# Performance work log

Hardware: AMD Instinct MI355X
Metric: run time of the kernel (lower is better)

## Reference

```python
import jax, jax.numpy as jnp
import numpy as np

B, S, D, H = 4, 1024, 1024, 16
HD = D // H  # 64
NEG = -10000000.0


def setup_inputs() -> dict:
    key = jax.random.key(0)
    ks = jax.random.split(key, 8)
    x = jax.random.normal(ks[0], (B, S, D), dtype=jnp.float32)
    adj = jax.random.randint(ks[1], (B, S, S), 0, 2).astype(jnp.float32)
    scale = 1.0 / np.sqrt(D)
    Wq = jax.random.normal(ks[2], (D, D), dtype=jnp.float32) * scale
    bq = jnp.zeros((D,), dtype=jnp.float32)
    Wk = jax.random.normal(ks[3], (D, D), dtype=jnp.float32) * scale
    bk = jnp.zeros((D,), dtype=jnp.float32)
    Wv = jax.random.normal(ks[4], (D, D), dtype=jnp.float32) * scale
    bv = jnp.zeros((D,), dtype=jnp.float32)
    return {"x": x, "adj": adj, "Wq": Wq, "bq": bq, "Wk": Wk, "bk": bk, "Wv": Wv, "bv": bv}


def reference(x, adj, Wq, bq, Wk, bk, Wv, bv):
    # QKV projections, split into heads: [B,S,D] -> [B,H,S,HD]
    def heads(t):
        return t.reshape(B, S, H, HD).transpose(0, 2, 1, 3)

    q = heads(x @ Wq + bq)
    k = heads(x @ Wk + bk)
    v = heads(x @ Wv + bv)

    # scaled scores [B,H,S,S]
    scores = jnp.einsum('bhqd,bhkd->bhqk', q, k) / jnp.sqrt(jnp.asarray(HD, x.dtype))
    # adjacency mask: 0 where adj>=0.5 else -1e7, broadcast over heads
    mask_add = jnp.where(adj < 0.5, jnp.asarray(NEG, x.dtype), jnp.asarray(0.0, x.dtype))
    scores = scores + mask_add[:, None, :, :]

    probs = jax.nn.softmax(scores, axis=-1)
    ctx = jnp.einsum('bhqk,bhkd->bhqd', probs, v)  # [B,H,S,HD]
    ctx = ctx.transpose(0, 2, 1, 3).reshape(B, S, D)
    h = jax.nn.relu(ctx)
    return (h, adj)
```

## Files before the change

### kernel.cpp

```cpp
#include <hip/hip_runtime.h>

constexpr int Bn  = 4;
constexpr int Sn  = 1024;
constexpr int Dn  = 1024;
constexpr int Hn  = 16;
constexpr int HDn = 64;

using short8   = __attribute__((ext_vector_type(8))) short;
using float4v  = __attribute__((ext_vector_type(4))) float;
using float16v = __attribute__((ext_vector_type(16))) float;

__device__ __forceinline__ ushort f2bf(float f) {
    union { float f; unsigned u; } v; v.f = f;
    unsigned r = v.u + 0x7fff + ((v.u >> 16) & 1);
    return (ushort)(r >> 16);
}

__device__ __forceinline__ void gload16(const void* g, void* l) {
    __builtin_amdgcn_global_load_lds(
        (const __attribute__((address_space(1))) void*)g,
        (__attribute__((address_space(3))) void*)l, 16, 0, 0);
}

__global__ __launch_bounds__(256) void prep(
    const float* __restrict__ x,
    const float* __restrict__ Wq, const float* __restrict__ Wk,
    const float* __restrict__ Wv, const float* __restrict__ adj,
    ushort* __restrict__ xb, ushort* __restrict__ Wt, uint* __restrict__ Mb,
    float* __restrict__ out)
{
    const int bx  = blockIdx.x;
    const int tid = threadIdx.x;
    __shared__ __align__(16) ushort pool[64 * 72];

    if (bx < 2048) {
        const size_t i = ((size_t)bx * 256 + tid) * 8;
        float4 a = *(const float4*)&x[i];
        float4 b = *(const float4*)&x[i + 4];
        ushort o[8] = {f2bf(a.x), f2bf(a.y), f2bf(a.z), f2bf(a.w),
                       f2bf(b.x), f2bf(b.y), f2bf(b.z), f2bf(b.w)};
        *(uint4*)&xb[i] = *(const uint4*)o;
    } else if (bx < 2816) {
        const int idx = bx - 2048;
        const int which = idx >> 8, rem = idx & 255;
        const float* __restrict__ W = (which == 0) ? Wq : (which == 1) ? Wk : Wv;
        ushort* __restrict__ O = Wt + (size_t)which * Dn * Dn;
        const int k0 = (rem & 15) * 64, n0 = (rem >> 4) * 64;
        ushort* T = pool;

        const int kl = tid >> 4, nl = (tid & 15) * 4;
#pragma unroll
        for (int p = 0; p < 4; ++p) {
            float4 w4 = *(const float4*)&W[(size_t)(k0 + p * 16 + kl) * Dn + n0 + nl];
            T[(nl + 0) * 72 + p * 16 + kl] = f2bf(w4.x);
            T[(nl + 1) * 72 + p * 16 + kl] = f2bf(w4.y);
            T[(nl + 2) * 72 + p * 16 + kl] = f2bf(w4.z);
            T[(nl + 3) * 72 + p * 16 + kl] = f2bf(w4.w);
        }
        __syncthreads();
        const int nr = tid >> 2, kc = (tid & 3) * 16;
        uint4 u0 = *(const uint4*)&T[nr * 72 + kc];
        uint4 u1 = *(const uint4*)&T[nr * 72 + kc + 8];
        *(uint4*)&O[(size_t)(n0 + nr) * Dn + k0 + kc]     = u0;
        *(uint4*)&O[(size_t)(n0 + nr) * Dn + k0 + kc + 8] = u1;
    } else {
        const int idx = bx - 2816;
        const int kt = idx & 15, qt = (idx >> 4) & 7, b = idx >> 7;
        char* msk = (char*)pool;

        float* ocopy = out + (size_t)Bn * Sn * Dn;
        const int r16 = tid >> 4, c4 = (tid & 15) * 4;
#pragma unroll
        for (int p = 0; p < 8; ++p) {
            const int row = p * 16 + r16;
            const size_t gi = ((size_t)b * Sn + qt * 128 + row) * Sn + kt * 64 + c4;
            float4 a = *(const float4*)&adj[gi];
            *(float4*)&ocopy[gi] = a;
            char* mr = &msk[row * 68 + c4];
            mr[0] = a.x >= 0.5f; mr[1] = a.y >= 0.5f;
            mr[2] = a.z >= 0.5f; mr[3] = a.w >= 0.5f;
        }
        __syncthreads();

        const int lane = tid & 63, w = tid >> 6;
        const int col = lane & 31, hi = lane >> 5;
        uint words[16];
#pragma unroll
        for (int mt = 0; mt < 2; ++mt)
#pragma unroll
            for (int pr = 0; pr < 8; ++pr) {
                const int r0 = 2 * pr;
                const int kl = mt * 32 + (r0 & 3) + 8 * (r0 >> 2) + 4 * hi;
                const char* mr = &msk[(w * 32 + col) * 68];
                words[mt * 8 + pr] = (mr[kl]     ? 0x0000FFFFu : 0u) |
                                     (mr[kl + 1] ? 0xFFFF0000u : 0u);
            }
        uint* dst = Mb + ((((size_t)(b * 8 + qt) * 16 + kt) * 4 + w) * 64 + lane) * 16;
#pragma unroll
        for (int c = 0; c < 4; ++c)
            *(uint4*)&dst[c * 4] =
                make_uint4(words[c*4], words[c*4+1], words[c*4+2], words[c*4+3]);
    }
}

__global__ __launch_bounds__(256) void qkv_gemm(
    const ushort* __restrict__ xb, const ushort* __restrict__ Wt,
    const float* __restrict__ bq, const float* __restrict__ bk,
    const float* __restrict__ bv,
    ushort* __restrict__ Qb, ushort* __restrict__ Kb, ushort* __restrict__ Vb)
{
    const int which = blockIdx.z;
    const ushort* __restrict__ Bw   = Wt + (size_t)which * Dn * Dn;
    const float* __restrict__  bias = (which == 0) ? bq : (which == 1) ? bk : bv;
    ushort* __restrict__       Out  = (which == 0) ? Qb : (which == 1) ? Kb : Vb;
    const float scale = (which == 0) ? 0.18033688011112042f : 1.0f;

    const int n0   = blockIdx.x * 128;
    const int m0   = blockIdx.y * 128;
    const int tid  = threadIdx.x;
    const int wave = tid >> 6;
    const int lane = tid & 63;
    const int wm   = wave >> 1;
    const int wn   = wave & 1;

    __shared__ __align__(16) ushort As[128 * 32];
    __shared__ __align__(16) ushort Bs[128 * 32];

    const int L0 = wave * 64 + lane;
    const int r0s = L0 >> 2, c0s = (L0 & 3) * 8;
    const int L1 = L0 + 256;
    const int r1s = L1 >> 2, c1s = (L1 & 3) * 8;

    const ushort* pA0 = &xb[(size_t)(m0 + r0s) * Dn + c0s];
    const ushort* pA1 = &xb[(size_t)(m0 + r1s) * Dn + c1s];
    const ushort* pB0 = &Bw[(size_t)(n0 + r0s) * Dn + c0s];
    const ushort* pB1 = &Bw[(size_t)(n0 + r1s) * Dn + c1s];

    char* ldsA0 = (char*)As + wave * 1024;
    char* ldsA1 = (char*)As + wave * 1024 + 4096;
    char* ldsB0 = (char*)Bs + wave * 1024;
    char* ldsB1 = (char*)Bs + wave * 1024 + 4096;

    const int mlane = lane & 15;
    const int kg    = (lane >> 4) * 8;

    float4v acc[4][4];
    const float4v z4 = {0.f, 0.f, 0.f, 0.f};
#pragma unroll
    for (int i = 0; i < 4; ++i)
#pragma unroll
        for (int j = 0; j < 4; ++j) acc[i][j] = z4;

    for (int k0 = 0; k0 < Dn; k0 += 32) {
        __syncthreads();
        gload16(pA0, ldsA0);
        gload16(pA1, ldsA1);
        gload16(pB0, ldsB0);
        gload16(pB1, ldsB1);
        pA0 += 32; pA1 += 32; pB0 += 32; pB1 += 32;
        __syncthreads();

        short8 af[4], bf[4];
#pragma unroll
        for (int i = 0; i < 4; ++i)
            af[i] = *(const short8*)&As[(wm * 64 + i * 16 + mlane) * 32 + kg];
#pragma unroll
        for (int j = 0; j < 4; ++j)
            bf[j] = *(const short8*)&Bs[(wn * 64 + j * 16 + mlane) * 32 + kg];
#pragma unroll
        for (int i = 0; i < 4; ++i)
#pragma unroll
            for (int j = 0; j < 4; ++j)
                acc[i][j] = __builtin_amdgcn_mfma_f32_16x16x32_bf16(af[i], bf[j], acc[i][j], 0, 0, 0);
    }

    const int rb  = (lane >> 4) * 4;
    const int col = lane & 15;
#pragma unroll
    for (int j = 0; j < 4; ++j) {
        const int n  = n0 + wn * 64 + j * 16 + col;
        const float bias_n = bias[n];
        const int h  = n >> 6;
        const int hd = n & 63;
#pragma unroll
        for (int i = 0; i < 4; ++i) {
#pragma unroll
            for (int r = 0; r < 4; ++r) {
                const int m = m0 + wm * 64 + i * 16 + rb + r;
                const int b = m >> 10;
                const int s = m & 1023;
                size_t addr;
                if (which == 2)
                    addr = (((size_t)(b * Hn + h)) * HDn + hd) * Sn + s;
                else
                    addr = (((size_t)(b * Hn + h)) * Sn + s) * HDn + hd;
                Out[addr] = f2bf((acc[i][j][r] + bias_n) * scale);
            }
        }
    }
}

__global__ __launch_bounds__(512, 4) void attn_mfma(
    const ushort* __restrict__ Q, const ushort* __restrict__ K,
    const ushort* __restrict__ Vt, const uint* __restrict__ Mw,
    float* __restrict__ out)
{
    const int n  = blockIdx.x;
    const int qt = (n >> 3) & 7;
    const int bh = (n & 7) | ((n >> 6) << 3);
    const int h  = bh & 15;
    const int b  = bh >> 4;

    const int tid  = threadIdx.x;
    const int w    = tid >> 6, lane = tid & 63;
    const int g    = w >> 2;
    const int wq   = w & 3;
    const int col  = lane & 31, hi = lane >> 5;

    const size_t hb = ((size_t)(b * Hn + h)) * Sn * HDn;
    const ushort* Kg = K + hb;
    const ushort* Vg = Vt + hb;

    __shared__ __align__(16) ushort KV[2][2][2][64 * 72];

    short8 qf[4];
#pragma unroll
    for (int kp = 0; kp < 4; ++kp)
        qf[kp] = *(const short8*)&Q[hb +
            (size_t)(qt * 128 + wq * 32 + col) * HDn + kp * 16 + hi * 8];

    float16v o_[2];
#pragma unroll
    for (int dt = 0; dt < 2; ++dt)
#pragma unroll
        for (int r = 0; r < 16; ++r) o_[dt][r] = 0.f;
    float ls = 0.f;

    const int t  = tid & 255;
    const int c0 = t, c1 = t + 256;
    const int la0 = (c0 >> 3) * 72 + (c0 & 7) * 8;
    const int la1 = (c1 >> 3) * 72 + (c1 & 7) * 8;
    const int kb  = g * 8;

    uint4 k0 = *(const uint4*)&Kg[(size_t)(kb * 64 + (c0 >> 3)) * HDn + (c0 & 7) * 8];
    uint4 k1 = *(const uint4*)&Kg[(size_t)(kb * 64 + (c1 >> 3)) * HDn + (c1 & 7) * 8];
    uint4 v0 = *(const uint4*)&Vg[(size_t)(c0 >> 3) * Sn + kb * 64 + (c0 & 7) * 8];
    uint4 v1 = *(const uint4*)&Vg[(size_t)(c1 >> 3) * Sn + kb * 64 + (c1 & 7) * 8];
    *(uint4*)&KV[g][0][0][la0] = k0;  *(uint4*)&KV[g][0][0][la1] = k1;
    *(uint4*)&KV[g][0][1][la0] = v0;  *(uint4*)&KV[g][0][1][la1] = v1;
    __syncthreads();

    const uint* mbase = Mw + ((size_t)((b * 8 + qt) * 16) * 4 + wq) * 1024 + lane * 16;

    for (int kt = 0; kt < 8; ++kt) {
        const int cur = kt & 1;
        if (kt < 7) {
            const int nk = (kb + kt + 1) * 64;
            k0 = *(const uint4*)&Kg[(size_t)(nk + (c0 >> 3)) * HDn + (c0 & 7) * 8];
            k1 = *(const uint4*)&Kg[(size_t)(nk + (c1 >> 3)) * HDn + (c1 & 7) * 8];
            v0 = *(const uint4*)&Vg[(size_t)(c0 >> 3) * Sn + nk + (c0 & 7) * 8];
            v1 = *(const uint4*)&Vg[(size_t)(c1 >> 3) * Sn + nk + (c1 & 7) * 8];
        }
        const uint* mp = mbase + (size_t)(kb + kt) * 4096;
        uint4 mk4[4];
        mk4[0] = *(const uint4*)(mp);
        mk4[1] = *(const uint4*)(mp + 4);
        mk4[2] = *(const uint4*)(mp + 8);
        mk4[3] = *(const uint4*)(mp + 12);
        const uint* mka = (const uint*)mk4;

#pragma unroll
        for (int mt = 0; mt < 2; ++mt) {
            float16v s_;
#pragma unroll
            for (int r = 0; r < 16; ++r) s_[r] = 0.f;
#pragma unroll
            for (int kp = 0; kp < 4; ++kp) {
                short8 ak = *(const short8*)&KV[g][cur][0][(mt * 32 + col) * 72 + kp * 16 + hi * 8];
                s_ = __builtin_amdgcn_mfma_f32_32x32x16_bf16(ak, qf[kp], s_, 0, 0, 0);
            }

            unsigned up[8];
#pragma unroll
            for (int pr = 0; pr < 8; ++pr) {
                const unsigned e0 = __float_as_uint(exp2f(s_[2 * pr]))     + 0x8000u;
                const unsigned e1 = __float_as_uint(exp2f(s_[2 * pr + 1])) + 0x8000u;
                const unsigned u  = __builtin_amdgcn_perm(e1, e0, 0x07060302u) & mka[mt * 8 + pr];
                up[pr] = u;
                ls += __uint_as_float(u << 16) + __uint_as_float(u & 0xffff0000u);
            }

#pragma unroll
            for (int kh = 0; kh < 2; ++kh) {
                const unsigned a0 = up[kh * 4 + 0], a1 = up[kh * 4 + 1];
                const unsigned a2 = up[kh * 4 + 2], a3 = up[kh * 4 + 3];
                const unsigned t0 = (unsigned)__shfl_xor((int)(hi ? a0 : a2), 32, 64);
                const unsigned t1 = (unsigned)__shfl_xor((int)(hi ? a1 : a3), 32, 64);
                union { short8 s; unsigned u[4]; } f;
                f.u[0] = hi ? t0 : a0;
                f.u[1] = hi ? t1 : a1;
                f.u[2] = hi ? a2 : t0;
                f.u[3] = hi ? a3 : t1;
                const int kp = mt * 2 + kh;
#pragma unroll
                for (int dt = 0; dt < 2; ++dt) {
                    short8 av = *(const short8*)&KV[g][cur][1][(dt * 32 + col) * 72 + kp * 16 + hi * 8];
                    o_[dt] = __builtin_amdgcn_mfma_f32_32x32x16_bf16(av, f.s, o_[dt], 0, 0, 0);
                }
            }
        }

        if (kt < 7) {
            const int nxt = cur ^ 1;
            *(uint4*)&KV[g][nxt][0][la0] = k0;  *(uint4*)&KV[g][nxt][0][la1] = k1;
            *(uint4*)&KV[g][nxt][1][la0] = v0;  *(uint4*)&KV[g][nxt][1][la1] = v1;
        }
        __syncthreads();
    }

    float* xo  = (float*)&KV[0][0][0][0];
    float* lsx = xo + 4 * 64 * 36;
    if (g == 1) {
        float* dst = &xo[(wq * 64 + lane) * 36];
#pragma unroll
        for (int dt = 0; dt < 2; ++dt)
#pragma unroll
            for (int r4 = 0; r4 < 4; ++r4) {
                float4 o4 = make_float4(o_[dt][r4 * 4 + 0], o_[dt][r4 * 4 + 1],
                                        o_[dt][r4 * 4 + 2], o_[dt][r4 * 4 + 3]);
                *(float4*)&dst[dt * 16 + r4 * 4] = o4;
            }
        lsx[wq * 64 + lane] = ls;
    }
    __syncthreads();
    if (g == 0) {
        const float* src = &xo[(wq * 64 + lane) * 36];
        const float lt = ls + lsx[wq * 64 + lane];
        const float l  = lt + (float)__shfl_xor(lt, 32, 64);
        const float inv = 1.0f / l;
        const int q = qt * 128 + wq * 32 + col;
        float* op = &out[((size_t)b * Sn + q) * Dn + h * 64];
#pragma unroll
        for (int dt = 0; dt < 2; ++dt)
#pragma unroll
            for (int rg = 0; rg < 4; ++rg) {
                float4 s4 = *(const float4*)&src[dt * 16 + rg * 4];
                const int d = dt * 32 + rg * 8 + hi * 4;
                float4 o4;
                o4.x = fmaxf((o_[dt][rg * 4 + 0] + s4.x) * inv, 0.0f);
                o4.y = fmaxf((o_[dt][rg * 4 + 1] + s4.y) * inv, 0.0f);
                o4.z = fmaxf((o_[dt][rg * 4 + 2] + s4.z) * inv, 0.0f);
                o4.w = fmaxf((o_[dt][rg * 4 + 3] + s4.w) * inv, 0.0f);
                *(float4*)&op[d] = o4;
            }
    }
}

extern "C" void kernel_launch(void* const* d_in, const int* in_sizes, int n_in,
                              void* d_out, int out_size, void* d_ws, size_t ws_size,
                              hipStream_t stream)
{
    const float* x   = (const float*)d_in[0];
    const float* adj = (const float*)d_in[1];
    const float* Wq  = (const float*)d_in[2];
    const float* bq  = (const float*)d_in[3];
    const float* Wk  = (const float*)d_in[4];
    const float* bk  = (const float*)d_in[5];
    const float* Wv  = (const float*)d_in[6];
    const float* bv  = (const float*)d_in[7];
    float* out = (float*)d_out;

    ushort* xb = (ushort*)d_ws;
    ushort* Wt = xb + (size_t)Bn * Sn * Dn;
    ushort* Qb = Wt + (size_t)3 * Dn * Dn;
    ushort* Kb = Qb + (size_t)Bn * Hn * Sn * HDn;
    ushort* Vb = Kb + (size_t)Bn * Hn * Sn * HDn;
    uint*   Mb = (uint*)(Vb + (size_t)Bn * Hn * Sn * HDn);

    prep<<<dim3(3328), 256, 0, stream>>>(x, Wq, Wk, Wv, adj, xb, Wt, Mb, out);

    qkv_gemm<<<dim3(Dn / 128, (Bn * Sn) / 128, 3), 256, 0, stream>>>(
        xb, Wt, bq, bk, bv, Qb, Kb, Vb);

    attn_mfma<<<dim3(512), 512, 0, stream>>>(Qb, Kb, Vb, Mb, out);
}
```

Before: 185.5 us.

## Swizzle GEMM LDS, remap block order, prefetch mask, use permlane32 swap

Several unrelated changes land together. The QKV GEMM now uses a 1D grid with an XCD-aware block remap so neighbouring tiles share an L2. Its LDS layout gets an XOR swizzle on both the global_load_lds writes and the fragment reads to cut bank conflicts. In attention, the adjacency mask words are prefetched one key tile ahead, shuffles are replaced with permlane32_swap, and s_setprio is raised around the MFMA sections. These changes target load latency, LDS conflicts and cross-lane data movement, at the cost of more registers and a more complex index mapping.

```diff
diff --git a/kernel.cpp b/kernel.cpp
--- a/kernel.cpp
+++ b/kernel.cpp
@@ -109,14 +109,20 @@
     const float* __restrict__ bv,
     ushort* __restrict__ Qb, ushort* __restrict__ Kb, ushort* __restrict__ Vb)
 {
-    const int which = blockIdx.z;
+    const int n  = blockIdx.x;
+    const int v  = (n & 7) * 96 + (n >> 3);
+    const int by = v / 24;
+    const int rr = v - by * 24;
+    const int bxi   = rr & 7;
+    const int which = rr >> 3;
+
     const ushort* __restrict__ Bw   = Wt + (size_t)which * Dn * Dn;
     const float* __restrict__  bias = (which == 0) ? bq : (which == 1) ? bk : bv;
     ushort* __restrict__       Out  = (which == 0) ? Qb : (which == 1) ? Kb : Vb;
     const float scale = (which == 0) ? 0.18033688011112042f : 1.0f;
 
-    const int n0   = blockIdx.x * 128;
-    const int m0   = blockIdx.y * 128;
+    const int n0   = bxi * 128;
+    const int m0   = by * 128;
     const int tid  = threadIdx.x;
     const int wave = tid >> 6;
     const int lane = tid & 63;
@@ -127,9 +133,9 @@
     __shared__ __align__(16) ushort Bs[128 * 32];
 
     const int L0 = wave * 64 + lane;
-    const int r0s = L0 >> 2, c0s = (L0 & 3) * 8;
+    const int r0s = L0 >> 2, c0s = ((L0 & 3) ^ ((L0 >> 3) & 3)) * 8;
     const int L1 = L0 + 256;
-    const int r1s = L1 >> 2, c1s = (L1 & 3) * 8;
+    const int r1s = L1 >> 2, c1s = ((L1 & 3) ^ ((L1 >> 3) & 3)) * 8;
 
     const ushort* pA0 = &xb[(size_t)(m0 + r0s) * Dn + c0s];
     const ushort* pA1 = &xb[(size_t)(m0 + r1s) * Dn + c1s];
@@ -142,7 +148,7 @@
     char* ldsB1 = (char*)Bs + wave * 1024 + 4096;
 
     const int mlane = lane & 15;
-    const int kg    = (lane >> 4) * 8;
+    const int kg = (((lane >> 4) ^ ((mlane >> 1) & 3))) * 8;
 
     float4v acc[4][4];
     const float4v z4 = {0.f, 0.f, 0.f, 0.f};
@@ -178,10 +184,10 @@
     const int col = lane & 15;
 #pragma unroll
     for (int j = 0; j < 4; ++j) {
-        const int n  = n0 + wn * 64 + j * 16 + col;
-        const float bias_n = bias[n];
-        const int h  = n >> 6;
-        const int hd = n & 63;
+        const int nn = n0 + wn * 64 + j * 16 + col;
+        const float bias_n = bias[nn];
+        const int h  = nn >> 6;
+        const int hd = nn & 63;
 #pragma unroll
         for (int i = 0; i < 4; ++i) {
 #pragma unroll
@@ -252,21 +258,30 @@
 
     const uint* mbase = Mw + ((size_t)((b * 8 + qt) * 16) * 4 + wq) * 1024 + lane * 16;
 
+    uint4 mk4[4];
+    {
+        const uint* mp = mbase + (size_t)kb * 4096;
+        mk4[0] = *(const uint4*)(mp);
+        mk4[1] = *(const uint4*)(mp + 4);
+        mk4[2] = *(const uint4*)(mp + 8);
+        mk4[3] = *(const uint4*)(mp + 12);
+    }
+
     for (int kt = 0; kt < 8; ++kt) {
         const int cur = kt & 1;
+        uint4 mn4[4];
         if (kt < 7) {
             const int nk = (kb + kt + 1) * 64;
             k0 = *(const uint4*)&Kg[(size_t)(nk + (c0 >> 3)) * HDn + (c0 & 7) * 8];
             k1 = *(const uint4*)&Kg[(size_t)(nk + (c1 >> 3)) * HDn + (c1 & 7) * 8];
             v0 = *(const uint4*)&Vg[(size_t)(c0 >> 3) * Sn + nk + (c0 & 7) * 8];
             v1 = *(const uint4*)&Vg[(size_t)(c1 >> 3) * Sn + nk + (c1 & 7) * 8];
-        }
-        const uint* mp = mbase + (size_t)(kb + kt) * 4096;
-        uint4 mk4[4];
-        mk4[0] = *(const uint4*)(mp);
-        mk4[1] = *(const uint4*)(mp + 4);
-        mk4[2] = *(const uint4*)(mp + 8);
-        mk4[3] = *(const uint4*)(mp + 12);
+            const uint* mp = mbase + (size_t)(kb + kt + 1) * 4096;
+            mn4[0] = *(const uint4*)(mp);
+            mn4[1] = *(const uint4*)(mp + 4);
+            mn4[2] = *(const uint4*)(mp + 8);
+            mn4[3] = *(const uint4*)(mp + 12);
+        }
         const uint* mka = (const uint*)mk4;
 
 #pragma unroll
@@ -274,11 +289,13 @@
             float16v s_;
 #pragma unroll
             for (int r = 0; r < 16; ++r) s_[r] = 0.f;
+            __builtin_amdgcn_s_setprio(1);
 #pragma unroll
             for (int kp = 0; kp < 4; ++kp) {
                 short8 ak = *(const short8*)&KV[g][cur][0][(mt * 32 + col) * 72 + kp * 16 + hi * 8];
                 s_ = __builtin_amdgcn_mfma_f32_32x32x16_bf16(ak, qf[kp], s_, 0, 0, 0);
             }
+            __builtin_amdgcn_s_setprio(0);
 
             unsigned up[8];
 #pragma unroll
@@ -290,17 +307,18 @@
                 ls += __uint_as_float(u << 16) + __uint_as_float(u & 0xffff0000u);
             }
 
+            __builtin_amdgcn_s_setprio(1);
 #pragma unroll
             for (int kh = 0; kh < 2; ++kh) {
-                const unsigned a0 = up[kh * 4 + 0], a1 = up[kh * 4 + 1];
-                const unsigned a2 = up[kh * 4 + 2], a3 = up[kh * 4 + 3];
-                const unsigned t0 = (unsigned)__shfl_xor((int)(hi ? a0 : a2), 32, 64);
-                const unsigned t1 = (unsigned)__shfl_xor((int)(hi ? a1 : a3), 32, 64);
+                auto s02 = __builtin_amdgcn_permlane32_swap(
+                    up[kh * 4 + 0], up[kh * 4 + 2], false, false);
+                auto s13 = __builtin_amdgcn_permlane32_swap(
+                    up[kh * 4 + 1], up[kh * 4 + 3], false, false);
                 union { short8 s; unsigned u[4]; } f;
-                f.u[0] = hi ? t0 : a0;
-                f.u[1] = hi ? t1 : a1;
-                f.u[2] = hi ? a2 : t0;
-                f.u[3] = hi ? a3 : t1;
+                f.u[0] = s02[0];
+                f.u[1] = s13[0];
+                f.u[2] = s02[1];
+                f.u[3] = s13[1];
                 const int kp = mt * 2 + kh;
 #pragma unroll
                 for (int dt = 0; dt < 2; ++dt) {
@@ -308,12 +326,14 @@
                     o_[dt] = __builtin_amdgcn_mfma_f32_32x32x16_bf16(av, f.s, o_[dt], 0, 0, 0);
                 }
             }
+            __builtin_amdgcn_s_setprio(0);
         }
 
         if (kt < 7) {
             const int nxt = cur ^ 1;
             *(uint4*)&KV[g][nxt][0][la0] = k0;  *(uint4*)&KV[g][nxt][0][la1] = k1;
             *(uint4*)&KV[g][nxt][1][la0] = v0;  *(uint4*)&KV[g][nxt][1][la1] = v1;
+            mk4[0] = mn4[0]; mk4[1] = mn4[1]; mk4[2] = mn4[2]; mk4[3] = mn4[3];
         }
         __syncthreads();
     }
@@ -379,8 +399,7 @@
 
     prep<<<dim3(3328), 256, 0, stream>>>(x, Wq, Wk, Wv, adj, xb, Wt, Mb, out);
 
-    qkv_gemm<<<dim3(Dn / 128, (Bn * Sn) / 128, 3), 256, 0, stream>>>(
-        xb, Wt, bq, bk, bv, Qb, Kb, Vb);
+    qkv_gemm<<<dim3(768), 256, 0, stream>>>(xb, Wt, bq, bk, bv, Qb, Kb, Vb);
 
     attn_mfma<<<dim3(512), 512, 0, stream>>>(Qb, Kb, Vb, Mb, out);
 }
```

Measured after the change: 212.5 us. 1.15x slower.
